# Kernel optimization log

Hardware: AMD Instinct MI355X
Metric: run time of the kernel (lower is better)

The kernel has to match this reference:

```python
import jax, jax.numpy as jnp
import numpy as np

B_, L_, D_, E_, N_, DR_, DC_ = 2, 2048, 1024, 2048, 16, 64, 4

def setup_inputs() -> dict:
    key = jax.random.key(0)
    ks = jax.random.split(key, 12)
    s = lambda fan: 1.0 / np.sqrt(fan)
    inp = {}
    inp['resid'] = jax.random.normal(ks[0], (B_, L_, D_), jnp.float32)
    inp['norm_w'] = jnp.ones((D_,), jnp.float32)
    inp['skip_w'] = jax.random.normal(ks[1], (E_, D_), jnp.float32) * s(D_)
    inp['in_w'] = jax.random.normal(ks[2], (E_, D_), jnp.float32) * s(D_)
    inp['conv_w'] = jax.random.normal(ks[3], (E_, DC_), jnp.float32) * s(DC_)
    inp['conv_b'] = jax.random.normal(ks[4], (E_,), jnp.float32) * 0.1
    inp['wd1'] = jax.random.normal(ks[5], (DR_, E_), jnp.float32) * s(E_)
    inp['wd2'] = jax.random.uniform(ks[6], (E_, DR_), jnp.float32, -1.0, 1.0) * (DR_ ** -0.5)
    # dt bias init: inverse softplus of dt in [dt_min, dt_max]
    dt = jnp.exp(jax.random.uniform(ks[7], (E_,), jnp.float32) * (np.log(0.1) - np.log(0.001)) + np.log(0.001))
    dt = jnp.clip(dt, 1e-4, None)
    inp['wd2_b'] = dt + jnp.log(-jnp.expm1(-dt))
    inp['wB'] = jax.random.normal(ks[8], (N_, E_), jnp.float32) * s(E_)
    inp['wC'] = jax.random.normal(ks[9], (N_, E_), jnp.float32) * s(E_)
    inp['A_log'] = jnp.log(jnp.broadcast_to(jnp.arange(1, N_ + 1, dtype=jnp.float32), (E_, N_)))
    inp['W_D'] = jnp.ones((E_,), jnp.float32)
    inp['out_w'] = jax.random.normal(ks[10], (D_, E_), jnp.float32) * s(E_)
    return inp


def reference(resid, norm_w, skip_w, in_w, conv_w, conv_b, wd1, wd2, wd2_b, wB, wC, A_log, W_D, out_w):
    eps = 1e-5
    # RMSNorm
    xn = resid * jax.lax.rsqrt(jnp.mean(resid * resid, axis=-1, keepdims=True) + eps) * norm_w
    skip = jnp.einsum('bld,ed->ble', xn, skip_w)          # [B,L,E]
    x = jnp.einsum('bld,ed->ble', xn, in_w)               # [B,L,E]
    # causal depthwise conv1d (padding d_conv-1, keep first L outputs)
    Dc = conv_w.shape[1]
    L = x.shape[1]
    xp = jnp.pad(x, ((0, 0), (Dc - 1, 0), (0, 0)))
    xc = conv_b + sum(xp[:, k:k + L, :] * conv_w[:, k] for k in range(Dc))
    x = jax.nn.silu(xc)                                   # ssm input [B,L,E]
    # input-dependent delta, B, C
    delta = jax.nn.softplus(jnp.einsum('blr,er->ble', jnp.einsum('ble,re->blr', x, wd1), wd2) + wd2_b)
    Bm = jnp.einsum('ble,ne->bln', x, wB)                 # [B,L,N]
    Cm = jnp.einsum('ble,ne->bln', x, wC)                 # [B,L,N]
    A = -jnp.exp(A_log)                                   # [E,N]
    # selective scan over L
    def step(h, inp):
        xt, dt, bt, ct = inp                              # [B,E],[B,E],[B,N],[B,N]
        h = jnp.exp(dt[:, :, None] * A) * h + (dt * xt)[:, :, None] * bt[:, None, :]
        y = jnp.einsum('ben,bn->be', h, ct)
        return h, y
    h0 = jnp.zeros((x.shape[0], A.shape[0], A.shape[1]), x.dtype)
    xs = (jnp.swapaxes(x, 0, 1), jnp.swapaxes(delta, 0, 1),
          jnp.swapaxes(Bm, 0, 1), jnp.swapaxes(Cm, 0, 1))
    _, ys = jax.lax.scan(step, h0, xs)                    # ys: [L,B,E]
    y = jnp.swapaxes(ys, 0, 1) + W_D * x                  # skip connection D*x
    y = y * jax.nn.silu(skip)                             # gate
    out = jnp.einsum('ble,de->bld', y, out_w)
    return resid + out
```

## Files before the change

kernel.cpp:

```cpp
#include <hip/hip_runtime.h>
#include <hip/hip_bf16.h>

#define B_ 2
#define L_ 2048
#define D_ 1024
#define E_ 2048
#define N_ 16
#define DR_ 64
#define DC_ 4
#define M_ (B_*L_)
#define SSEG 16
#define LSEG (L_/SSEG)
#define KS_ 8
#define CH 32
#define LOG2E 1.4426950408889634f

typedef __attribute__((ext_vector_type(8))) short bf16x8;
typedef __attribute__((ext_vector_type(4))) float f32x4;

__device__ __forceinline__ ushort f2bf(float x){
    union { float f; unsigned u; } v; v.f = x;
    unsigned r = v.u + 0x7FFFu + ((v.u >> 16) & 1u);
    return (ushort)(r >> 16);
}
__device__ __forceinline__ float bf2f(ushort u){
    union { unsigned u; float f; } v; v.u = ((unsigned)u) << 16;
    return v.f;
}
__device__ __forceinline__ float fexp2(float x){
    float r;
    asm("v_exp_f32 %0, %1" : "=v"(r) : "v"(x));
    return r;
}
__device__ __forceinline__ float fast_silu(float x){
    return x * __builtin_amdgcn_rcpf(1.f + __expf(-x));
}
__device__ __forceinline__ float softplus_f(float z){
    return (z > 20.f) ? z : __logf(1.f + __expf(z));
}

#define DPP_F(x, CTRL) __int_as_float(__builtin_amdgcn_update_dpp(0, __float_as_int(x), (CTRL), 0xf, 0xf, true))

__device__ __forceinline__ void gld16(const void* g, void* l){
    __builtin_amdgcn_global_load_lds(
        (const __attribute__((address_space(1))) unsigned int*)g,
        (__attribute__((address_space(3))) unsigned int*)l,
        16, 0, 0);
}

#define PR0 (E_*D_/4)
#define PR1 (2*PR0)
#define PR2 (3*PR0)
#define PR3 (PR2 + E_*DR_/4)
#define PR4 (PR3 + DR_*E_/4)
#define PR5 (PR4 + N_*E_/4)
#define PR6 (PR5 + N_*E_/4)
#define PR7 (PR6 + 32*E_/4)
#define PR8 (PR7 + 4*E_/4)
__global__ __launch_bounds__(256) void prep_k(const float* __restrict__ in_w,
                                              const float* __restrict__ skip_w,
                                              const float* __restrict__ out_w,
                                              const float* __restrict__ wd2,
                                              const float* __restrict__ wd1,
                                              const float* __restrict__ wB,
                                              const float* __restrict__ wC,
                                              const float* __restrict__ conv_w,
                                              ushort* __restrict__ wis,
                                              ushort* __restrict__ wo,
                                              ushort* __restrict__ wd2b,
                                              ushort* __restrict__ W96,
                                              float* __restrict__ cwT){
    int i = blockIdx.x * 256 + threadIdx.x;
    const float* src; ushort* dst; int off;
    if (i < PR0)      { src = in_w;   dst = wis;                       off = i; }
    else if (i < PR1) { src = skip_w; dst = wis + (size_t)E_*D_;       off = i - PR0; }
    else if (i < PR2) { src = out_w;  dst = wo;                        off = i - PR1; }
    else if (i < PR3) { src = wd2;    dst = wd2b;                      off = i - PR2; }
    else if (i < PR4) { src = wd1;    dst = W96;                       off = i - PR3; }
    else if (i < PR5) { src = wB;     dst = W96 + (size_t)64*E_;       off = i - PR4; }
    else if (i < PR6) { src = wC;     dst = W96 + (size_t)80*E_;       off = i - PR5; }
    else if (i < PR7) {
        ushort4 z = {0,0,0,0};
        ((ushort4*)(W96 + (size_t)96*E_))[i - PR6] = z;
        return;
    } else if (i < PR8) {
        int u = i - PR7;
        int k = u >> 9;
        int g = u & 511;
        float4 o;
        o.x = conv_w[(g*4 + 0)*4 + k];
        o.y = conv_w[(g*4 + 1)*4 + k];
        o.z = conv_w[(g*4 + 2)*4 + k];
        o.w = conv_w[(g*4 + 3)*4 + k];
        ((float4*)(cwT + (size_t)k * E_))[g] = o;
        return;
    } else return;
    float4 v = ((const float4*)src)[off];
    ushort4 o;
    o.x = f2bf(v.x); o.y = f2bf(v.y); o.z = f2bf(v.z); o.w = f2bf(v.w);
    ((ushort4*)dst)[off] = o;
}

__global__ __launch_bounds__(256) void rmsnorm_k(const float* __restrict__ resid,
                                                 const float* __restrict__ norm_w,
                                                 ushort* __restrict__ xn){
    int row = blockIdx.x;
    const float4* r = (const float4*)(resid + (size_t)row * D_);
    float4 v = r[threadIdx.x];
    float ss = v.x*v.x + v.y*v.y + v.z*v.z + v.w*v.w;
    for (int m = 32; m; m >>= 1) ss += __shfl_xor(ss, m);
    __shared__ float sred[4];
    if ((threadIdx.x & 63) == 0) sred[threadIdx.x >> 6] = ss;
    __syncthreads();
    float tot = sred[0] + sred[1] + sred[2] + sred[3];
    float scale = rsqrtf(tot / (float)D_ + 1e-5f);
    const float4* wv = (const float4*)norm_w;
    float4 w = wv[threadIdx.x];
    ushort4 o;
    o.x = f2bf(v.x * scale * w.x);
    o.y = f2bf(v.y * scale * w.y);
    o.z = f2bf(v.z * scale * w.z);
    o.w = f2bf(v.w * scale * w.w);
    ((ushort4*)(xn + (size_t)row * D_))[threadIdx.x] = o;
}

#define BM 128
#define BN 128
#define BK 64

__global__ __launch_bounds__(512, 4)
void gemm_dual_k(const ushort* __restrict__ A, const ushort* __restrict__ Bm,
                 ushort* __restrict__ P1, ushort* __restrict__ P2){
    __shared__ __align__(16) ushort As[2][BM * BK];
    __shared__ __align__(16) ushort Bs[2][BN * BK];
    const int xcd = blockIdx.x & 7;
    const int idx = blockIdx.x >> 3;
    const int row0 = (((xcd >> 2) << 4) + (idx >> 3)) * BM;
    const int col0 = (((xcd & 3) << 3) + (idx & 7)) * BN;
    const int tid = threadIdx.x;
    const int lane = tid & 63;
    const int wid = tid >> 6;
    const int wm = wid >> 1, wn = wid & 1;
    f32x4 acc[2][4] = {};
    const int l8 = lane >> 3;
    const int cs = ((lane & 7) ^ (l8 & 7)) * 8;

    const int NK = D_ / BK;
    #pragma unroll
    for (int i = 0; i < 2; ++i){
        const int R0 = wid * 16 + i * 8;
        gld16(A + (size_t)(row0 + R0 + l8) * D_ + cs, &As[0][R0 * BK]);
        gld16(Bm + (size_t)(col0 + R0 + l8) * D_ + cs, &Bs[0][R0 * BK]);
    }
    __syncthreads();
    int cur = 0;
    for (int ki = 0; ki < NK; ++ki){
        if (ki + 1 < NK){
            const int k0 = (ki + 1) * BK;
            #pragma unroll
            for (int i = 0; i < 2; ++i){
                const int R0 = wid * 16 + i * 8;
                gld16(A + (size_t)(row0 + R0 + l8) * D_ + k0 + cs, &As[cur^1][R0 * BK]);
                gld16(Bm + (size_t)(col0 + R0 + l8) * D_ + k0 + cs, &Bs[cur^1][R0 * BK]);
            }
        }
        #pragma unroll
        for (int kk = 0; kk < 2; ++kk){
            bf16x8 af[2], bfr[4];
            const int krow = lane & 15;
            const int kcol = ((kk * 4 + (lane >> 4)) ^ (krow & 7)) * 8;
            #pragma unroll
            for (int mi = 0; mi < 2; ++mi)
                af[mi] = *(const bf16x8*)(&As[cur][(wm*32 + mi*16 + krow) * BK + kcol]);
            #pragma unroll
            for (int ni = 0; ni < 4; ++ni)
                bfr[ni] = *(const bf16x8*)(&Bs[cur][(wn*64 + ni*16 + krow) * BK + kcol]);
            #pragma unroll
            for (int mi = 0; mi < 2; ++mi)
                #pragma unroll
                for (int ni = 0; ni < 4; ++ni)
                    acc[mi][ni] = __builtin_amdgcn_mfma_f32_16x16x32_bf16(af[mi], bfr[ni], acc[mi][ni], 0, 0, 0);
        }
        __syncthreads();
        cur ^= 1;
    }
    ushort* base = (col0 < E_) ? P1 : P2;
    const int cb = (col0 < E_) ? col0 : col0 - E_;
    #pragma unroll
    for (int mi = 0; mi < 2; ++mi)
        #pragma unroll
        for (int ni = 0; ni < 4; ++ni)
            #pragma unroll
            for (int j = 0; j < 4; ++j){
                int r = row0 + wm*32 + mi*16 + (lane >> 4) * 4 + j;
                int c = cb + wn*64 + ni*16 + (lane & 15);
                base[(size_t)r * E_ + c] = f2bf(acc[mi][ni][j]);
            }
}

#define OBM 64
__global__ __launch_bounds__(512, 4)
void gemm_out_k(const ushort* __restrict__ A, const ushort* __restrict__ Bm,
                float* __restrict__ Cp, const float* __restrict__ aux){
    __shared__ __align__(16) ushort As[2][OBM * BK];
    __shared__ __align__(16) ushort Bs[2][BN * BK];
    const int wid9 = (blockIdx.x & 7) * 64 + (blockIdx.x >> 3);
    const int col0 = (wid9 & 7) * BN;
    const int row0 = (wid9 >> 3) * OBM;
    const int tid = threadIdx.x;
    const int lane = tid & 63;
    const int wid = tid >> 6;
    const int wm = wid >> 1, wn = wid & 1;
    f32x4 acc[4] = {};
    const int l8 = lane >> 3;
    const int cs = ((lane & 7) ^ (l8 & 7)) * 8;

    const int NK = E_ / BK;
    {
        const int R0a = wid * 8;
        gld16(A + (size_t)(row0 + R0a + l8) * E_ + cs, &As[0][R0a * BK]);
        #pragma unroll
        for (int i = 0; i < 2; ++i){
            const int R0 = wid * 16 + i * 8;
            gld16(Bm + (size_t)(col0 + R0 + l8) * E_ + cs, &Bs[0][R0 * BK]);
        }
    }
    __syncthreads();
    int cur = 0;
    for (int ki = 0; ki < NK; ++ki){
        if (ki + 1 < NK){
            const int k0 = (ki + 1) * BK;
            const int R0a = wid * 8;
            gld16(A + (size_t)(row0 + R0a + l8) * E_ + k0 + cs, &As[cur^1][R0a * BK]);
            #pragma unroll
            for (int i = 0; i < 2; ++i){
                const int R0 = wid * 16 + i * 8;
                gld16(Bm + (size_t)(col0 + R0 + l8) * E_ + k0 + cs, &Bs[cur^1][R0 * BK]);
            }
        }
        #pragma unroll
        for (int kk = 0; kk < 2; ++kk){
            bf16x8 af, bfr[4];
            const int krow = lane & 15;
            const int kcol = ((kk * 4 + (lane >> 4)) ^ (krow & 7)) * 8;
            af = *(const bf16x8*)(&As[cur][(wm*16 + krow) * BK + kcol]);
            #pragma unroll
            for (int ni = 0; ni < 4; ++ni)
                bfr[ni] = *(const bf16x8*)(&Bs[cur][(wn*64 + ni*16 + krow) * BK + kcol]);
            #pragma unroll
            for (int ni = 0; ni < 4; ++ni)
                acc[ni] = __builtin_amdgcn_mfma_f32_16x16x32_bf16(af, bfr[ni], acc[ni], 0, 0, 0);
        }
        __syncthreads();
        cur ^= 1;
    }
    #pragma unroll
    for (int ni = 0; ni < 4; ++ni)
        #pragma unroll
        for (int j = 0; j < 4; ++j){
            int r = row0 + wm*16 + (lane >> 4) * 4 + j;
            int c = col0 + wn*64 + ni*16 + (lane & 15);
            size_t idx = (size_t)r * D_ + c;
            Cp[idx] = acc[ni][j] + aux[idx];
        }
}

#define CBM 64
__global__ __launch_bounds__(512, 4)
void gemm_c96_sk(const ushort* __restrict__ A, const ushort* __restrict__ Bm,
                 float* __restrict__ part){
    __shared__ __align__(16) ushort As[CBM * BK];
    __shared__ __align__(16) ushort Bs[128 * BK];
    const int ks = blockIdx.x;
    const int row0 = blockIdx.y * CBM;
    const int tid = threadIdx.x;
    const int lane = tid & 63;
    const int wid = tid >> 6;
    const int wm = wid >> 1, wn = wid & 1;
    f32x4 acc[4] = {};
    const int l8 = lane >> 3;
    const int cs = ((lane & 7) ^ (l8 & 7)) * 8;

    for (int k0 = ks * (E_ / KS_); k0 < (ks + 1) * (E_ / KS_); k0 += BK){
        {
            const int R0a = wid * 8;
            gld16(A + (size_t)(row0 + R0a + l8) * E_ + k0 + cs, As + R0a * BK);
            #pragma unroll
            for (int i = 0; i < 2; ++i){
                const int R0 = wid * 16 + i * 8;
                gld16(Bm + (size_t)(R0 + l8) * E_ + k0 + cs, Bs + R0 * BK);
            }
        }
        __syncthreads();
        #pragma unroll
        for (int kk = 0; kk < 2; ++kk){
            bf16x8 af, bfr[4];
            const int krow = lane & 15;
            const int kcol = ((kk * 4 + (lane >> 4)) ^ (krow & 7)) * 8;
            af = *(const bf16x8*)(As + (wm*16 + krow) * BK + kcol);
            #pragma unroll
            for (int ni = 0; ni < 4; ++ni)
                bfr[ni] = *(const bf16x8*)(Bs + (wn*64 + ni*16 + krow) * BK + kcol);
            #pragma unroll
            for (int ni = 0; ni < 4; ++ni)
                acc[ni] = __builtin_amdgcn_mfma_f32_16x16x32_bf16(af, bfr[ni], acc[ni], 0, 0, 0);
        }
        __syncthreads();
    }
    float* dst = part + (size_t)ks * M_ * 128;
    #pragma unroll
    for (int ni = 0; ni < 4; ++ni)
        #pragma unroll
        for (int j = 0; j < 4; ++j){
            int r = row0 + wm*16 + (lane >> 4) * 4 + j;
            int c = wn*64 + ni*16 + (lane & 15);
            dst[(size_t)r * 128 + c] = acc[ni][j];
        }
}

__global__ __launch_bounds__(256) void c96_reduce_k(const float* __restrict__ part,
                                                    ushort* __restrict__ C96){
    int i4 = blockIdx.x * 256 + threadIdx.x;
    float4 a = *(const float4*)(part + (size_t)i4 * 4);
    #pragma unroll
    for (int k = 1; k < KS_; ++k){
        float4 b = *(const float4*)(part + (size_t)k * M_ * 128 + (size_t)i4 * 4);
        a.x += b.x; a.y += b.y; a.z += b.z; a.w += b.w;
    }
    ushort4 o;
    o.x = f2bf(a.x); o.y = f2bf(a.y); o.z = f2bf(a.z); o.w = f2bf(a.w);
    *(ushort4*)(C96 + (size_t)i4 * 4) = o;
}

__global__ __launch_bounds__(256) void conv_silu_k(const ushort* __restrict__ xpre,
                                                   const float* __restrict__ cwT,
                                                   const float* __restrict__ conv_b,
                                                   ushort* __restrict__ xb){
    int i4 = blockIdx.x * 256 + threadIdx.x;
    if (i4 >= M_ * E_ / 4) return;
    int idx = i4 * 4;
    int e = idx & (E_ - 1);
    int bl = idx >> 11;
    int t = bl & (L_ - 1);
    float4 b4 = *(const float4*)(conv_b + e);
    float a0 = b4.x, a1 = b4.y, a2 = b4.z, a3 = b4.w;
    #pragma unroll
    for (int k = 0; k < 4; ++k){
        int dt = 3 - k;
        if (t >= dt){
            ushort4 xv = *(const ushort4*)(xpre + idx - dt * E_);
            float4 wv = *(const float4*)(cwT + (size_t)k * E_ + e);
            a0 += bf2f(xv.x) * wv.x;
            a1 += bf2f(xv.y) * wv.y;
            a2 += bf2f(xv.z) * wv.z;
            a3 += bf2f(xv.w) * wv.w;
        }
    }
    ushort4 sb;
    sb.x = f2bf(fast_silu(a0));
    sb.y = f2bf(fast_silu(a1));
    sb.z = f2bf(fast_silu(a2));
    sb.w = f2bf(fast_silu(a3));
    *(ushort4*)(xb + idx) = sb;
}

#define SF2 36
#define SYD 20

__device__ __forceinline__ void seg_swz(int& b, int& s, int& e0){
    int lin = blockIdx.x + 128 * (blockIdx.y + 16 * blockIdx.z);
    int swz = (lin & 7) * 512 + (lin >> 3);
    e0 = (swz & 127) * 16;
    s  = (swz >> 7) & 15;
    b  = swz >> 11;
}

__global__ __launch_bounds__(256, 8) void seg1_k(const ushort* __restrict__ xb,
                                              const ushort* __restrict__ C96,
                                              const ushort* __restrict__ wd2b,
                                              const float* __restrict__ wd2_bias,
                                              const float* __restrict__ A_log,
                                              float* __restrict__ F,
                                              float* __restrict__ segdt){
    int b, s, e0; seg_swz(b, s, e0);
    const int tid = threadIdx.x;
    const int lane = tid & 63, wid = tid >> 6;
    const int n = tid & 15, ei = tid >> 4;
    const int e = e0 + ei;
    const float Aen2 = -__expf(A_log[e * N_ + n]) * LOG2E;
    float h = 0.f;
    __shared__ __align__(16) ushort sxr[CH][72];
    __shared__ __align__(16) ushort swd2[16][72];
    __shared__ __align__(16) ushort sxu[16][40];
    __shared__ float sd[16][SF2], sdx[16][SF2], sB[16][SF2];
    __shared__ float ssdt[2][16];
    const int tq = tid >> 3, qc = tid & 7;

    if (tid < 128){
        int r = tid >> 3, cc = (tid & 7) * 8;
        *(uint4*)&swd2[r][cc] = *(const uint4*)(wd2b + (size_t)(e0 + r) * DR_ + cc);
    }
    const float bias = wd2_bias[e0 + (lane & 15)];
    float psdt = 0.f;

    for (int c = 0; c < LSEG / CH; ++c){
        int t0 = s * LSEG + c * CH;
        size_t row = (size_t)(b * L_ + t0 + tq);
        *(uint4*)&sxr[tq][qc * 8] = *(const uint4*)(C96 + row * 128 + qc * 8);
        ushort2 rB = *(const ushort2*)(C96 + row * 128 + 64 + qc * 2);
        ushort2 xu = *(const ushort2*)(xb + row * E_ + e0 + qc * 2);
        sB[qc*2+0][tq] = bf2f(rB.x); sB[qc*2+1][tq] = bf2f(rB.y);
        sxu[qc*2+0][tq] = xu.x; sxu[qc*2+1][tq] = xu.y;
        __syncthreads();
        if (wid < 2){
            f32x4 dacc = {};
            #pragma unroll
            for (int kk = 0; kk < 2; ++kk){
                bf16x8 af = *(const bf16x8*)&sxr[wid*16 + (lane & 15)][kk*32 + (lane >> 4)*8];
                bf16x8 bf = *(const bf16x8*)&swd2[lane & 15][kk*32 + (lane >> 4)*8];
                dacc = __builtin_amdgcn_mfma_f32_16x16x32_bf16(af, bf, dacc, 0, 0, 0);
            }
            const int crow = lane & 15;
            const int ttc = wid*16 + (lane >> 4)*4;
            float4 dv;
            dv.x = softplus_f(dacc[0] + bias);
            dv.y = softplus_f(dacc[1] + bias);
            dv.z = softplus_f(dacc[2] + bias);
            dv.w = softplus_f(dacc[3] + bias);
            *(float4*)&sd[crow][ttc] = dv;
            psdt += dv.x + dv.y + dv.z + dv.w;
            ushort4 xu4 = *(const ushort4*)&sxu[crow][ttc];
            float4 dxv;
            dxv.x = dv.x * bf2f(xu4.x); dxv.y = dv.y * bf2f(xu4.y);
            dxv.z = dv.z * bf2f(xu4.z); dxv.w = dv.w * bf2f(xu4.w);
            *(float4*)&sdx[crow][ttc] = dxv;
        }
        __syncthreads();
        #pragma unroll
        for (int t = 0; t < CH; t += 4){
            float4 d4  = *(const float4*)&sd[ei][t];
            float4 dx4 = *(const float4*)&sdx[ei][t];
            float4 b4  = *(const float4*)&sB[n][t];
            h = fexp2(d4.x*Aen2)*h + dx4.x*b4.x;
            h = fexp2(d4.y*Aen2)*h + dx4.y*b4.y;
            h = fexp2(d4.z*Aen2)*h + dx4.z*b4.z;
            h = fexp2(d4.w*Aen2)*h + dx4.w*b4.w;
        }
        __syncthreads();
    }
    if (wid < 2){
        psdt += __shfl_xor(psdt, 16);
        psdt += __shfl_xor(psdt, 32);
        if (lane < 16) ssdt[wid][lane] = psdt;
    }
    size_t base = ((size_t)(b * SSEG + s) * E_ + e) * N_ + n;
    F[base] = h;
    __syncthreads();
    if (tid < 16)
        segdt[(size_t)(b * SSEG + s) * E_ + e0 + tid] = ssdt[0][tid] + ssdt[1][tid];
}

__global__ __launch_bounds__(256) void carry_k(const float* __restrict__ F,
                                               const float* __restrict__ segdt,
                                               const float* __restrict__ A_log,
                                               float* __restrict__ carr){
    int idx = blockIdx.x * 256 + threadIdx.x;
    int n = idx & 15;
    int e = (idx >> 4) & (E_ - 1);
    int b = idx >> 15;
    const float Aen2 = -__expf(A_log[e * N_ + n]) * LOG2E;
    float c = 0.f;
    #pragma unroll
    for (int s = 0; s < SSEG; ++s){
        size_t base = ((size_t)(b * SSEG + s) * E_ + e) * N_ + n;
        carr[base] = c;
        float P = fexp2(Aen2 * segdt[(size_t)(b * SSEG + s) * E_ + e]);
        c = P * c + F[base];
    }
}

__global__ __launch_bounds__(256, 8) void seg2_k(const ushort* __restrict__ xb,
                                              const ushort* __restrict__ C96,
                                              const ushort* __restrict__ wd2b,
                                              const float* __restrict__ wd2_bias,
                                              const float* __restrict__ A_log,
                                              const float* __restrict__ carr,
                                              const ushort* __restrict__ skipb,
                                              const float* __restrict__ W_D,
                                              ushort* __restrict__ y2){
    int b, s, e0; seg_swz(b, s, e0);
    const int tid = threadIdx.x;
    const int lane = tid & 63, wid = tid >> 6;
    const int n = tid & 15, ei = tid >> 4;
    const int e = e0 + ei;
    const float Aen2 = -__expf(A_log[e * N_ + n]) * LOG2E;
    float h = carr[((size_t)(b * SSEG + s) * E_ + e) * N_ + n];
    __shared__ __align__(16) ushort sxr[CH][72];
    __shared__ __align__(16) ushort swd2[16][72];
    __shared__ __align__(16) ushort sxu[16][40];
    __shared__ float sd[16][SF2], sdx[16][SF2], sB[16][SF2], sC[16][SF2];
    __shared__ float sy[CH][SYD];
    const int tq = tid >> 3, qc = tid & 7;

    if (tid < 128){
        int r = tid >> 3, cc = (tid & 7) * 8;
        *(uint4*)&swd2[r][cc] = *(const uint4*)(wd2b + (size_t)(e0 + r) * DR_ + cc);
    }
    const float bias = wd2_bias[e0 + (lane & 15)];
    const float wv0 = W_D[e0 + qc * 2], wv1 = W_D[e0 + qc * 2 + 1];

    for (int c = 0; c < LSEG / CH; ++c){
        int t0 = s * LSEG + c * CH;
        size_t row = (size_t)(b * L_ + t0 + tq);
        *(uint4*)&sxr[tq][qc * 8] = *(const uint4*)(C96 + row * 128 + qc * 8);
        ushort2 rB = *(const ushort2*)(C96 + row * 128 + 64 + qc * 2);
        ushort2 rC = *(const ushort2*)(C96 + row * 128 + 80 + qc * 2);
        ushort2 xu = *(const ushort2*)(xb + row * E_ + e0 + qc * 2);
        ushort2 sv_pre = *(const ushort2*)(skipb + row * E_ + e0 + qc * 2);
        sB[qc*2+0][tq] = bf2f(rB.x); sB[qc*2+1][tq] = bf2f(rB.y);
        sC[qc*2+0][tq] = bf2f(rC.x); sC[qc*2+1][tq] = bf2f(rC.y);
        sxu[qc*2+0][tq] = xu.x; sxu[qc*2+1][tq] = xu.y;
        __syncthreads();
        if (wid < 2){
            f32x4 dacc = {};
            #pragma unroll
            for (int kk = 0; kk < 2; ++kk){
                bf16x8 af = *(const bf16x8*)&sxr[wid*16 + (lane & 15)][kk*32 + (lane >> 4)*8];
                bf16x8 bf = *(const bf16x8*)&swd2[lane & 15][kk*32 + (lane >> 4)*8];
                dacc = __builtin_amdgcn_mfma_f32_16x16x32_bf16(af, bf, dacc, 0, 0, 0);
            }
            const int crow = lane & 15;
            const int ttc = wid*16 + (lane >> 4)*4;
            float4 dv;
            dv.x = softplus_f(dacc[0] + bias);
            dv.y = softplus_f(dacc[1] + bias);
            dv.z = softplus_f(dacc[2] + bias);
            dv.w = softplus_f(dacc[3] + bias);
            *(float4*)&sd[crow][ttc] = dv;
            ushort4 xu4 = *(const ushort4*)&sxu[crow][ttc];
            float4 dxv;
            dxv.x = dv.x * bf2f(xu4.x); dxv.y = dv.y * bf2f(xu4.y);
            dxv.z = dv.z * bf2f(xu4.z); dxv.w = dv.w * bf2f(xu4.w);
            *(float4*)&sdx[crow][ttc] = dxv;
        }
        __syncthreads();
        #pragma unroll
        for (int t = 0; t < CH; t += 4){
            float4 d4  = *(const float4*)&sd[ei][t];
            float4 dx4 = *(const float4*)&sdx[ei][t];
            float4 b4  = *(const float4*)&sB[n][t];
            float4 c4  = *(const float4*)&sC[n][t];
            float y0, y1, y2v, y3;
            h = fexp2(d4.x*Aen2)*h + dx4.x*b4.x;  y0 = h * c4.x;
            h = fexp2(d4.y*Aen2)*h + dx4.y*b4.y;  y1 = h * c4.y;
            h = fexp2(d4.z*Aen2)*h + dx4.z*b4.z;  y2v = h * c4.z;
            h = fexp2(d4.w*Aen2)*h + dx4.w*b4.w;  y3 = h * c4.w;
            float s01 = (n & 1) ? y0 : y1;
            float r01 = DPP_F(s01, 0xB1);
            float s23 = (n & 1) ? y2v : y3;
            float r23 = DPP_F(s23, 0xB1);
            float va, vb;
            if (n & 1){ va = y1 + r01; vb = y3 + r23; }
            else      { va = y0 + r01; vb = y2v + r23; }
            float s2 = (n & 2) ? va : vb;
            float r2 = DPP_F(s2, 0x4E);
            float v = ((n & 2) ? vb : va) + r2;
            v += DPP_F(v, 0x124);
            v += DPP_F(v, 0x128);
            if (n < 4) sy[t + n][ei] = v;
        }
        __syncthreads();
        {
            size_t orow = (size_t)(b * L_ + t0 + tq);
            float yv0 = sy[tq][qc*2], yv1 = sy[tq][qc*2+1];
            float xs0 = bf2f(sxu[qc*2+0][tq]), xs1 = bf2f(sxu[qc*2+1][tq]);
            float sk0 = bf2f(sv_pre.x), sk1 = bf2f(sv_pre.y);
            ushort2 o;
            o.x = f2bf((yv0 + wv0 * xs0) * fast_silu(sk0));
            o.y = f2bf((yv1 + wv1 * xs1) * fast_silu(sk1));
            *(ushort2*)(y2 + orow * E_ + e0 + qc * 2) = o;
        }
        __syncthreads();
    }
}

extern "C" void kernel_launch(void* const* d_in, const int* in_sizes, int n_in,
                              void* d_out, int out_size, void* d_ws, size_t ws_size,
                              hipStream_t stream){
    const float* resid  = (const float*)d_in[0];
    const float* norm_w = (const float*)d_in[1];
    const float* skip_w = (const float*)d_in[2];
    const float* in_w   = (const float*)d_in[3];
    const float* conv_w = (const float*)d_in[4];
    const float* conv_b = (const float*)d_in[5];
    const float* wd1    = (const float*)d_in[6];
    const float* wd2    = (const float*)d_in[7];
    const float* wd2_b  = (const float*)d_in[8];
    const float* wB     = (const float*)d_in[9];
    const float* wC     = (const float*)d_in[10];
    const float* A_log  = (const float*)d_in[11];
    const float* W_D    = (const float*)d_in[12];
    const float* out_w  = (const float*)d_in[13];
    float* out = (float*)d_out;

    char* ws = (char*)d_ws;
    size_t off = 0;
    auto alloc = [&](size_t bytes) -> char* {
        char* p = ws + off;
        off += (bytes + 255) & ~(size_t)255;
        return p;
    };
    char* alias_base = ws;
    ushort* wis_b   = (ushort*)alloc((size_t)2 * E_ * D_ * 2);
    ushort* xn_b    = (ushort*)alloc((size_t)M_ * D_ * 2);
    ushort* xpre_b  = (ushort*)alloc((size_t)M_ * E_ * 2);
    float*  part_buf= (float*)alias_base;
    ushort* wo_b    = (ushort*)alloc((size_t)D_ * E_ * 2);
    ushort* wd2_bf  = (ushort*)alloc((size_t)E_ * DR_ * 2);
    ushort* W96_b   = (ushort*)alloc((size_t)128 * E_ * 2);
    float*  cwT_b   = (float*)alloc((size_t)4 * E_ * 4);
    ushort* skip_b  = (ushort*)alloc((size_t)M_ * E_ * 2);
    ushort* xb_b    = (ushort*)alloc((size_t)M_ * E_ * 2);
    ushort* C96_b   = (ushort*)alloc((size_t)M_ * 128 * 2);
    float*  scr     = (float*)alloc((size_t)9 * 1024 * 1024);
    ushort* y2_b    = (ushort*)alloc((size_t)M_ * E_ * 2);
    float* F_buf    = scr;
    float* carr_buf = scr + (size_t)B_ * SSEG * E_ * N_;
    float* segdt_buf= scr + (size_t)2 * B_ * SSEG * E_ * N_;
    (void)ws_size; (void)in_sizes; (void)n_in; (void)out_size;

    const int thr = 256;

    prep_k<<<(PR8 + 255)/256, thr, 0, stream>>>(in_w, skip_w, out_w, wd2, wd1, wB, wC, conv_w,
                                                wis_b, wo_b, wd2_bf, W96_b, cwT_b);

    rmsnorm_k<<<M_, thr, 0, stream>>>(resid, norm_w, xn_b);

    gemm_dual_k<<<1024, 512, 0, stream>>>(xn_b, wis_b, xpre_b, skip_b);

    conv_silu_k<<<(M_*E_/4 + 255)/256, thr, 0, stream>>>(xpre_b, cwT_b, conv_b, xb_b);

    gemm_c96_sk<<<dim3(KS_, M_/CBM), 512, 0, stream>>>(xb_b, W96_b, part_buf);
    c96_reduce_k<<<(M_*128/4)/256, thr, 0, stream>>>(part_buf, C96_b);

    seg1_k<<<dim3(E_/16, SSEG, B_), thr, 0, stream>>>(xb_b, C96_b, wd2_bf, wd2_b, A_log, F_buf, segdt_buf);
    carry_k<<<(B_*E_*N_)/256, thr, 0, stream>>>(F_buf, segdt_buf, A_log, carr_buf);
    seg2_k<<<dim3(E_/16, SSEG, B_), thr, 0, stream>>>(xb_b, C96_b, wd2_bf, wd2_b, A_log, carr_buf,
                                                      skip_b, W_D, y2_b);

    gemm_out_k<<<512, 512, 0, stream>>>(y2_b, wo_b, out, resid);
}
```

Baseline: 191.5 us.

## Triple-buffer LDS in dual and output GEMMs with partial vmcnt barriers

Converts the double-buffered LDS K-loop in the fused skip/in-projection GEMM and the output-projection GEMM to a three-stage ring. Each iteration prefetches two tiles ahead and waits only on the older loads via s_waitcnt vmcnt(N) plus a raw barrier, instead of a full __syncthreads. This is meant to hide more global-load latency behind the MFMA work. It raises LDS use (the dual GEMM drops its occupancy hint from 4 to 2 blocks) and depends on the hand-counted vmcnt values being right.

```diff
diff --git a/kernel.cpp b/kernel.cpp
--- a/kernel.cpp
+++ b/kernel.cpp
@@ -47,6 +47,12 @@
         (__attribute__((address_space(3))) unsigned int*)l,
         16, 0, 0);
 }
+
+#define PIPE_BAR(N) do { \
+    asm volatile("s_waitcnt vmcnt(" #N ")" ::: "memory"); \
+    __builtin_amdgcn_s_barrier(); \
+    __builtin_amdgcn_sched_barrier(0); \
+} while(0)
 
 #define PR0 (E_*D_/4)
 #define PR1 (2*PR0)
@@ -128,11 +134,11 @@
 #define BN 128
 #define BK 64
 
-__global__ __launch_bounds__(512, 4)
+__global__ __launch_bounds__(512, 2)
 void gemm_dual_k(const ushort* __restrict__ A, const ushort* __restrict__ Bm,
                  ushort* __restrict__ P1, ushort* __restrict__ P2){
-    __shared__ __align__(16) ushort As[2][BM * BK];
-    __shared__ __align__(16) ushort Bs[2][BN * BK];
+    __shared__ __align__(16) ushort As[3][BM * BK];
+    __shared__ __align__(16) ushort Bs[3][BN * BK];
     const int xcd = blockIdx.x & 7;
     const int idx = blockIdx.x >> 3;
     const int row0 = (((xcd >> 2) << 4) + (idx >> 3)) * BM;
@@ -152,16 +158,23 @@
         gld16(A + (size_t)(row0 + R0 + l8) * D_ + cs, &As[0][R0 * BK]);
         gld16(Bm + (size_t)(col0 + R0 + l8) * D_ + cs, &Bs[0][R0 * BK]);
     }
-    __syncthreads();
-    int cur = 0;
+    #pragma unroll
+    for (int i = 0; i < 2; ++i){
+        const int R0 = wid * 16 + i * 8;
+        gld16(A + (size_t)(row0 + R0 + l8) * D_ + BK + cs, &As[1][R0 * BK]);
+        gld16(Bm + (size_t)(col0 + R0 + l8) * D_ + BK + cs, &Bs[1][R0 * BK]);
+    }
+    PIPE_BAR(4);
     for (int ki = 0; ki < NK; ++ki){
-        if (ki + 1 < NK){
-            const int k0 = (ki + 1) * BK;
+        const int cur = ki % 3;
+        if (ki + 2 < NK){
+            const int k0 = (ki + 2) * BK;
+            const int nb = (ki + 2) % 3;
             #pragma unroll
             for (int i = 0; i < 2; ++i){
                 const int R0 = wid * 16 + i * 8;
-                gld16(A + (size_t)(row0 + R0 + l8) * D_ + k0 + cs, &As[cur^1][R0 * BK]);
-                gld16(Bm + (size_t)(col0 + R0 + l8) * D_ + k0 + cs, &Bs[cur^1][R0 * BK]);
+                gld16(A + (size_t)(row0 + R0 + l8) * D_ + k0 + cs, &As[nb][R0 * BK]);
+                gld16(Bm + (size_t)(col0 + R0 + l8) * D_ + k0 + cs, &Bs[nb][R0 * BK]);
             }
         }
         #pragma unroll
@@ -181,8 +194,10 @@
                 for (int ni = 0; ni < 4; ++ni)
                     acc[mi][ni] = __builtin_amdgcn_mfma_f32_16x16x32_bf16(af[mi], bfr[ni], acc[mi][ni], 0, 0, 0);
         }
-        __syncthreads();
-        cur ^= 1;
+        if (ki + 1 < NK){
+            if (ki + 2 < NK) PIPE_BAR(4);
+            else             PIPE_BAR(0);
+        }
     }
     ushort* base = (col0 < E_) ? P1 : P2;
     const int cb = (col0 < E_) ? col0 : col0 - E_;
@@ -202,8 +217,8 @@
 __global__ __launch_bounds__(512, 4)
 void gemm_out_k(const ushort* __restrict__ A, const ushort* __restrict__ Bm,
                 float* __restrict__ Cp, const float* __restrict__ aux){
-    __shared__ __align__(16) ushort As[2][OBM * BK];
-    __shared__ __align__(16) ushort Bs[2][BN * BK];
+    __shared__ __align__(16) ushort As[3][OBM * BK];
+    __shared__ __align__(16) ushort Bs[3][BN * BK];
     const int wid9 = (blockIdx.x & 7) * 64 + (blockIdx.x >> 3);
     const int col0 = (wid9 & 7) * BN;
     const int row0 = (wid9 >> 3) * OBM;
@@ -216,26 +231,29 @@
     const int cs = ((lane & 7) ^ (l8 & 7)) * 8;
 
     const int NK = E_ / BK;
-    {
+    #pragma unroll
+    for (int t = 0; t < 2; ++t){
+        const int k0 = t * BK;
         const int R0a = wid * 8;
-        gld16(A + (size_t)(row0 + R0a + l8) * E_ + cs, &As[0][R0a * BK]);
+        gld16(A + (size_t)(row0 + R0a + l8) * E_ + k0 + cs, &As[t][R0a * BK]);
         #pragma unroll
         for (int i = 0; i < 2; ++i){
             const int R0 = wid * 16 + i * 8;
-            gld16(Bm + (size_t)(col0 + R0 + l8) * E_ + cs, &Bs[0][R0 * BK]);
-        }
-    }
-    __syncthreads();
-    int cur = 0;
+            gld16(Bm + (size_t)(col0 + R0 + l8) * E_ + k0 + cs, &Bs[t][R0 * BK]);
+        }
+    }
+    PIPE_BAR(3);
     for (int ki = 0; ki < NK; ++ki){
-        if (ki + 1 < NK){
-            const int k0 = (ki + 1) * BK;
+        const int cur = ki % 3;
+        if (ki + 2 < NK){
+            const int k0 = (ki + 2) * BK;
+            const int nb = (ki + 2) % 3;
             const int R0a = wid * 8;
-            gld16(A + (size_t)(row0 + R0a + l8) * E_ + k0 + cs, &As[cur^1][R0a * BK]);
+            gld16(A + (size_t)(row0 + R0a + l8) * E_ + k0 + cs, &As[nb][R0a * BK]);
             #pragma unroll
             for (int i = 0; i < 2; ++i){
                 const int R0 = wid * 16 + i * 8;
-                gld16(Bm + (size_t)(col0 + R0 + l8) * E_ + k0 + cs, &Bs[cur^1][R0 * BK]);
+                gld16(Bm + (size_t)(col0 + R0 + l8) * E_ + k0 + cs, &Bs[nb][R0 * BK]);
             }
         }
         #pragma unroll
@@ -251,8 +269,10 @@
             for (int ni = 0; ni < 4; ++ni)
                 acc[ni] = __builtin_amdgcn_mfma_f32_16x16x32_bf16(af, bfr[ni], acc[ni], 0, 0, 0);
         }
-        __syncthreads();
-        cur ^= 1;
+        if (ki + 1 < NK){
+            if (ki + 2 < NK) PIPE_BAR(3);
+            else             PIPE_BAR(0);
+        }
     }
     #pragma unroll
     for (int ni = 0; ni < 4; ++ni)
```

Measured after the change: 203.2 us. +6.1%, slower.
